# Kernel tuning notes

Measured on AMD Instinct MI355X. Metric: run time of the kernel, lower is better.

Reference implementation:

```python
import jax, jax.numpy as jnp
import numpy as np

THETA = 10000.0


def apply_rope(x, theta):
    # x: [batch, heads, seq, head_dim], head_dim even
    d = x.shape[-1]
    s = x.shape[-2]
    freqs = 1.0 / (theta ** (jnp.arange(0, d, 2, dtype=jnp.float32) / d))  # [d/2]
    pos = jnp.arange(s, dtype=jnp.float32)
    ang = pos[:, None] * freqs[None, :]          # [seq, d/2]
    cos, sin = jnp.cos(ang), jnp.sin(ang)
    x_even = x[..., 0::2]
    x_odd = x[..., 1::2]
    r_even = x_even * cos - x_odd * sin
    r_odd = x_even * sin + x_odd * cos
    # interleave back: [..., seq, d/2, 2] -> [..., seq, d]
    out = jnp.stack([r_even, r_odd], axis=-1).reshape(x.shape)
    return out


def setup_inputs() -> dict:
    key = jax.random.key(0)
    ks = jax.random.split(key, 5)
    B, S, D = 2, 2048, 1024
    scale = 1.0 / np.sqrt(D)
    return {
        "x": jax.random.normal(ks[0], (B, S, D), dtype=jnp.float32),
        "q_proj_weight": jax.random.normal(ks[1], (D, D), dtype=jnp.float32) * scale,
        "k_proj_weight": jax.random.normal(ks[2], (D, D), dtype=jnp.float32) * scale,
        "v_proj_weight": jax.random.normal(ks[3], (D, D), dtype=jnp.float32) * scale,
        "o_proj_weight": jax.random.normal(ks[4], (D, D), dtype=jnp.float32) * scale,
    }


def reference(x, q_proj_weight, k_proj_weight, v_proj_weight, o_proj_weight):
    B, S, D = x.shape
    H = 16
    hd = D // H
    # projections: weight is (d_out, d_in)
    q = jnp.einsum('bsd,ed->bse', x, q_proj_weight)
    k = jnp.einsum('bsd,ed->bse', x, k_proj_weight)
    v = jnp.einsum('bsd,ed->bse', x, v_proj_weight)
    # split heads -> [B, H, S, hd]
    q = q.reshape(B, S, H, hd).transpose(0, 2, 1, 3)
    k = k.reshape(B, S, H, hd).transpose(0, 2, 1, 3)
    v = v.reshape(B, S, H, hd).transpose(0, 2, 1, 3)
    q = apply_rope(q, THETA)
    k = apply_rope(k, THETA)
    scores = jnp.einsum('bhqd,bhkd->bhqk', q, k) / jnp.sqrt(jnp.float32(hd))
    causal = jnp.tril(jnp.ones((S, S), dtype=bool))
    scores = jnp.where(causal, scores, -jnp.inf)
    attn = jax.nn.softmax(scores, axis=-1)
    out = jnp.einsum('bhqk,bhkd->bhqd', attn, v)
    out = out.transpose(0, 2, 1, 3).reshape(B, S, D)
    return jnp.einsum('bsv,dv->bsd', out, o_proj_weight)
```

## Files before the change

kernel.cpp:

```cpp
#include <hip/hip_runtime.h>
#include <hip/hip_bf16.h>
#include <stdint.h>

typedef __attribute__((ext_vector_type(4))) float f32x4;
typedef __attribute__((ext_vector_type(8))) __bf16 bf16x8;
typedef __attribute__((ext_vector_type(4))) __bf16 bf16x4;

#define DEVI __device__ __forceinline__

static constexpr int S_  = 2048;
static constexpr int D_  = 1024;
static constexpr int H_  = 16;
static constexpr int HD_ = 64;
static constexpr int M_  = 2 * S_;
static constexpr float SCL2 = 0.18033688f;

DEVI void gload_lds16(const void* gsrc, void* ldst) {
  __builtin_amdgcn_global_load_lds(
      (__attribute__((address_space(1))) void*)(void*)gsrc,
      (__attribute__((address_space(3))) void*)ldst, 16, 0, 0);
}

DEVI float fexp2(float x) {
  float r;
  asm("v_exp_f32 %0, %1" : "=v"(r) : "v"(x));
  return r;
}

__global__ __launch_bounds__(256) void cvt_all_kernel(
    const float* __restrict__ x, const float* __restrict__ wq,
    const float* __restrict__ wk, const float* __restrict__ wv,
    const float* __restrict__ wo,
    __bf16* __restrict__ xb, __bf16* __restrict__ wqb,
    __bf16* __restrict__ wkb, __bf16* __restrict__ wvb,
    __bf16* __restrict__ wob, float* __restrict__ tab) {
  int blk = blockIdx.x;
  if (blk < 8192) {
    int i = blk * 256 + threadIdx.x;
    const float* src; __bf16* dst; int off;
    if (i < (1 << 20))                      { src = x;  dst = xb;  off = 0; }
    else if (i < (1 << 20) + (1 << 18))     { src = wq; dst = wqb; off = (1 << 20); }
    else if (i < (1 << 20) + 2 * (1 << 18)) { src = wk; dst = wkb; off = (1 << 20) + (1 << 18); }
    else if (i < (1 << 20) + 3 * (1 << 18)) { src = wv; dst = wvb; off = (1 << 20) + 2 * (1 << 18); }
    else                                    { src = wo; dst = wob; off = (1 << 20) + 3 * (1 << 18); }
    int j = i - off;
    float4 v = reinterpret_cast<const float4*>(src)[j];
    bf16x4 o;
    o[0] = (__bf16)v.x; o[1] = (__bf16)v.y; o[2] = (__bf16)v.z; o[3] = (__bf16)v.w;
    reinterpret_cast<bf16x4*>(dst)[j] = o;
  } else {
    int i = (blk - 8192) * 256 + threadIdx.x;
    int s = i >> 5, f = i & 31;
    float freq = powf(10000.0f, -(float)(2 * f) / (float)HD_);
    float ang = (float)s * freq;
    tab[2 * i]     = cosf(ang);
    tab[2 * i + 1] = sinf(ang);
  }
}

__global__ __launch_bounds__(512, 6) void gemm_qkv(
    const __bf16* __restrict__ A, const __bf16* __restrict__ W0,
    const __bf16* __restrict__ W1, const __bf16* __restrict__ W2,
    __bf16* __restrict__ Cq, __bf16* __restrict__ Ck, __bf16* __restrict__ Cvt,
    const float* __restrict__ tab) {
  __shared__ __attribute__((aligned(16))) __bf16 As[128 * 32];
  __shared__ __attribute__((aligned(16))) __bf16 Bs[128 * 32];
  const int tid  = threadIdx.x;
  const int lane = tid & 63;
  const int wv   = tid >> 6;
  const int wr   = wv >> 2;
  const int wc   = wv & 3;
  const int m0 = blockIdx.x * 128;
  const int n0 = blockIdx.y * 128;
  const int z  = blockIdx.z;
  const __bf16* W = (z == 0) ? W0 : (z == 1 ? W1 : W2);
  const int arow = lane & 15;
  const int kgrp = (lane >> 4) * 8;

  f32x4 acc[4][2];
#pragma unroll
  for (int i = 0; i < 4; i++)
#pragma unroll
    for (int j = 0; j < 2; j++) acc[i][j] = f32x4{0.f, 0.f, 0.f, 0.f};

  for (int k0 = 0; k0 < 1024; k0 += 32) {
    __syncthreads();
    {
      int c   = wv * 64 + lane;
      int row = c >> 2;
      int kc  = (c & 3) * 8;
      gload_lds16(A + (size_t)(m0 + row) * 1024 + k0 + kc, As + wv * 512);
      gload_lds16(W + (size_t)(n0 + row) * 1024 + k0 + kc, Bs + wv * 512);
    }
    asm volatile("s_waitcnt vmcnt(0)" ::: "memory");
    __syncthreads();
    bf16x8 af[4], bw[2];
#pragma unroll
    for (int i = 0; i < 4; i++)
      af[i] = *reinterpret_cast<const bf16x8*>(As + (wr * 64 + i * 16 + arow) * 32 + kgrp);
#pragma unroll
    for (int j = 0; j < 2; j++)
      bw[j] = *reinterpret_cast<const bf16x8*>(Bs + (wc * 32 + j * 16 + arow) * 32 + kgrp);
#pragma unroll
    for (int i = 0; i < 4; i++)
#pragma unroll
      for (int j = 0; j < 2; j++)
        acc[i][j] = __builtin_amdgcn_mfma_f32_16x16x32_bf16(af[i], bw[j], acc[i][j], 0, 0, 0);
  }

  if (z == 2) {
#pragma unroll
    for (int i = 0; i < 4; i++) {
      int m = m0 + wr * 64 + i * 16 + (lane >> 4) * 4;
      int bb = m >> 11, srow = m & (S_ - 1);
#pragma unroll
      for (int j = 0; j < 2; j++) {
        int n = n0 + wc * 32 + j * 16 + arow;
        int h = n >> 6, d = n & 63;
        bf16x4 o4;
#pragma unroll
        for (int r = 0; r < 4; r++) o4[r] = (__bf16)acc[i][j][r];
        *reinterpret_cast<bf16x4*>(
            Cvt + ((size_t)(bb * H_ + h) * HD_ + d) * S_ + srow) = o4;
      }
    }
  } else {
#pragma unroll
    for (int i = 0; i < 4; i++) {
#pragma unroll
      for (int j = 0; j < 2; j++) {
#pragma unroll
        for (int r = 0; r < 4; r++) {
          int m = m0 + wr * 64 + i * 16 + (lane >> 4) * 4 + r;
          int n = n0 + wc * 32 + j * 16 + arow;
          float v = acc[i][j][r];
          int bb = m >> 11, srow = m & (S_ - 1);
          int h = n >> 6, d = n & 63;
          size_t oidx = ((size_t)(bb * H_ + h) * S_ + srow) * HD_ + d;
          float other = __shfl_xor(v, 1, 64);
          int fq = d >> 1;
          float2 cssn = *reinterpret_cast<const float2*>(tab + (srow * 32 + fq) * 2);
          float rv = (d & 1) ? (other * cssn.y + v * cssn.x)
                             : (v * cssn.x - other * cssn.y);
          if (z == 0) rv *= SCL2;
          ((z == 0) ? Cq : Ck)[oidx] = (__bf16)rv;
        }
      }
    }
  }
}

__global__ __launch_bounds__(512, 4) void gemm_bt0(
    const __bf16* __restrict__ A, const __bf16* __restrict__ W0,
    float* __restrict__ Cf) {
  __shared__ __attribute__((aligned(16))) __bf16 As[128 * 32];
  __shared__ __attribute__((aligned(16))) __bf16 Bs[64 * 32];
  const int tid  = threadIdx.x;
  const int lane = tid & 63;
  const int wv   = tid >> 6;
  const int wr   = wv >> 1;
  const int wc   = wv & 1;
  const int m0 = blockIdx.x * 128;
  const int n0 = blockIdx.y * 64;
  const int arow = lane & 15;
  const int kgrp = (lane >> 4) * 8;

  f32x4 acc[2][2];
#pragma unroll
  for (int i = 0; i < 2; i++)
#pragma unroll
    for (int j = 0; j < 2; j++) acc[i][j] = f32x4{0.f, 0.f, 0.f, 0.f};

  for (int k0 = 0; k0 < 1024; k0 += 32) {
    __syncthreads();
    {
      int c   = wv * 64 + lane;
      int row = c >> 2;
      int kc  = (c & 3) * 8;
      gload_lds16(A + (size_t)(m0 + row) * 1024 + k0 + kc, As + wv * 512);
      if (wv < 4)
        gload_lds16(W0 + (size_t)(n0 + row) * 1024 + k0 + kc, Bs + wv * 512);
    }
    asm volatile("s_waitcnt vmcnt(0)" ::: "memory");
    __syncthreads();
    bf16x8 af[2], bw[2];
#pragma unroll
    for (int i = 0; i < 2; i++)
      af[i] = *reinterpret_cast<const bf16x8*>(As + (wr * 32 + i * 16 + arow) * 32 + kgrp);
#pragma unroll
    for (int j = 0; j < 2; j++)
      bw[j] = *reinterpret_cast<const bf16x8*>(Bs + (wc * 32 + j * 16 + arow) * 32 + kgrp);
#pragma unroll
    for (int i = 0; i < 2; i++)
#pragma unroll
      for (int j = 0; j < 2; j++)
        acc[i][j] = __builtin_amdgcn_mfma_f32_16x16x32_bf16(af[i], bw[j], acc[i][j], 0, 0, 0);
  }

#pragma unroll
  for (int i = 0; i < 2; i++)
#pragma unroll
    for (int j = 0; j < 2; j++)
#pragma unroll
      for (int r = 0; r < 4; r++) {
        int m = m0 + wr * 32 + i * 16 + (lane >> 4) * 4 + r;
        int n = n0 + wc * 32 + j * 16 + arow;
        Cf[(size_t)m * D_ + n] = acc[i][j][r];
      }
}

__global__ __launch_bounds__(512, 4) void attn_kernel(
    const __bf16* __restrict__ Q, const __bf16* __restrict__ K,
    const __bf16* __restrict__ Vt, __bf16* __restrict__ O) {
  __shared__ __attribute__((aligned(16))) __bf16 Ks[2][128 * 64];
  __shared__ __attribute__((aligned(16))) __bf16 Vs[2][64 * 128];
  const int tid = threadIdx.x, lane = tid & 63, wv = tid >> 6;
  const int id   = blockIdx.x;
  const int half = id >> 8;
  const int sub  = id & 255;
  const int bh   = sub & 31;
  const int pr   = sub >> 5;
  const int qt   = half ? pr : 15 - pr;
  const int b = bh >> 4, h = bh & 15;
  const __bf16* Qb  = Q  + (size_t)bh * S_ * HD_;
  const __bf16* Kb  = K  + (size_t)bh * S_ * HD_;
  const __bf16* Vtb = Vt + (size_t)bh * HD_ * S_;
  const int arow = lane & 15, g = lane >> 4;

#define STAGE(K0, BK_, BV_)                                                   \
  do {                                                                        \
    _Pragma("unroll") for (int j = 0; j < 2; ++j) {                           \
      int c = (wv * 2 + j) * 64 + lane;                    \
      int rowk = c >> 3, qqk = c & 7;                                         \
      int qsk = qqk ^ (rowk & 7);                                             \
      int ctp = rowk >> 4, rw = rowk & 15;                                    \
      int kph = ((ctp & 4) << 4) + ((ctp & 2) << 4) + ((ctp & 1) << 2)        \
                + ((rw >> 2) << 3) + (rw & 3);                                \
      gload_lds16(Kb + (size_t)((K0) + kph) * HD_ + qsk * 8,                  \
                  (BK_) + (size_t)(wv * 2 + j) * 512);                        \
      int rowv = c >> 4, qqv = c & 15;                                        \
      int qsv = qqv ^ (rowv & 7);                                             \
      gload_lds16(Vtb + (size_t)rowv * S_ + (K0) + qsv * 8,                   \
                  (BV_) + (size_t)(wv * 2 + j) * 512);                        \
    }                                                                         \
  } while (0)

  const int q0 = qt * 128;
  const int nkv = qt + 1;
  const int qw = q0 + wv * 16;
  const int qg = qw + arow;

  bf16x8 aq[2];
#pragma unroll
  for (int j = 0; j < 2; j++)
    aq[j] = *reinterpret_cast<const bf16x8*>(
        Qb + (size_t)(qw + arow) * HD_ + j * 32 + g * 8);

  f32x4 po[4];
#pragma unroll
  for (int dt = 0; dt < 4; dt++) po[dt] = f32x4{0.f, 0.f, 0.f, 0.f};
  float mrow = -1e30f, lrow = 0.f;

  STAGE(0, Ks[0], Vs[0]);
  {
    int t1 = (nkv > 1) ? 128 : 0;
    STAGE(t1, Ks[1], Vs[1]);
  }
  asm volatile("s_waitcnt vmcnt(4)" ::: "memory");
  __builtin_amdgcn_s_barrier();

  for (int kt = 0; kt < nkv; ++kt) {
    const int k0 = kt * 128;
    const int cur = kt & 1;
    const __bf16* Kc = Ks[cur];
    const __bf16* Vc = Vs[cur];

    f32x4 sc4[8];
    __builtin_amdgcn_s_setprio(1);
#pragma unroll
    for (int ct = 0; ct < 8; ct++) {
      sc4[ct] = f32x4{0.f, 0.f, 0.f, 0.f};
      int L = ct * 16 + arow;
#pragma unroll
      for (int j2 = 0; j2 < 2; j2++) {
        int byt = (L * 128 + j2 * 64 + g * 16) ^ ((L & 7) << 4);
        bf16x8 kb = *reinterpret_cast<const bf16x8*>((const char*)Kc + byt);
        sc4[ct] = __builtin_amdgcn_mfma_f32_16x16x32_bf16(kb, aq[j2], sc4[ct], 0, 0, 0);
      }
    }
    __builtin_amdgcn_s_setprio(0);

    if (kt == nkv - 1) {
#pragma unroll
      for (int ct = 0; ct < 8; ct++) {
        int kb0 = k0 + ((ct & 4) << 4) + ((ct & 2) << 4) + ((ct & 1) << 2) + g * 8;
#pragma unroll
        for (int r = 0; r < 4; r++)
          if (kb0 + r > qg) sc4[ct][r] = -1e30f;
      }
    }

    float mc[8];
#pragma unroll
    for (int ct = 0; ct < 8; ct++)
      mc[ct] = fmaxf(fmaxf(sc4[ct][0], sc4[ct][1]),
                     fmaxf(sc4[ct][2], sc4[ct][3]));
#pragma unroll
    for (int sstep = 4; sstep > 0; sstep >>= 1)
#pragma unroll
      for (int ct = 0; ct < sstep; ct++) mc[ct] = fmaxf(mc[ct], mc[ct + sstep]);
    float mx = mc[0];
    mx = fmaxf(mx, __shfl_xor(mx, 16, 64));
    mx = fmaxf(mx, __shfl_xor(mx, 32, 64));

    bool noskip = !__all(mx <= mrow + 11.0f);
    if (noskip) {
      float mnew = fmaxf(mrow, mx);
      float corr = fexp2(mrow - mnew);
      mrow = mnew;
      lrow *= corr;
#pragma unroll
      for (int dt = 0; dt < 4; dt++)
#pragma unroll
        for (int r = 0; r < 4; r++) po[dt][r] *= corr;
    }

    float rc[8];
#pragma unroll
    for (int ct = 0; ct < 8; ct++) {
      float e0 = fexp2(sc4[ct][0] - mrow);
      float e1 = fexp2(sc4[ct][1] - mrow);
      float e2 = fexp2(sc4[ct][2] - mrow);
      float e3 = fexp2(sc4[ct][3] - mrow);
      sc4[ct][0] = e0; sc4[ct][1] = e1; sc4[ct][2] = e2; sc4[ct][3] = e3;
      rc[ct] = (e0 + e1) + (e2 + e3);
    }
#pragma unroll
    for (int sstep = 4; sstep > 0; sstep >>= 1)
#pragma unroll
      for (int ct = 0; ct < sstep; ct++) rc[ct] += rc[ct + sstep];
    float rs = rc[0];
    rs += __shfl_xor(rs, 16, 64);
    rs += __shfl_xor(rs, 32, 64);
    lrow += rs;

    bf16x8 pb[4];
#pragma unroll
    for (int h2 = 0; h2 < 2; h2++)
#pragma unroll
      for (int j2 = 0; j2 < 2; j2++) {
#pragma unroll
        for (int r = 0; r < 4; r++) {
          pb[h2 * 2 + j2][r]     = (__bf16)sc4[h2 * 4 + 2 * j2][r];
          pb[h2 * 2 + j2][4 + r] = (__bf16)sc4[h2 * 4 + 2 * j2 + 1][r];
        }
      }

    __builtin_amdgcn_s_setprio(1);
#pragma unroll
    for (int dt = 0; dt < 4; dt++) {
      int d = dt * 16 + arow;
#pragma unroll
      for (int jj = 0; jj < 4; jj++) {
        int byv = (d * 256 + jj * 64 + g * 16) ^ ((d & 7) << 4);
        bf16x8 vb = *reinterpret_cast<const bf16x8*>((const char*)Vc + byv);
        po[dt] = __builtin_amdgcn_mfma_f32_16x16x32_bf16(vb, pb[jj], po[dt], 0, 0, 0);
      }
    }
    __builtin_amdgcn_s_setprio(0);

    __builtin_amdgcn_s_barrier();
    if (kt < nkv - 1) {
      int nx = kt + 2;
      if (nx > nkv - 1) nx = nkv - 1;
      STAGE(nx * 128, Ks[cur], Vs[cur]);
      asm volatile("s_waitcnt vmcnt(4)" ::: "memory");
    } else {
      asm volatile("s_waitcnt vmcnt(0)" ::: "memory");
    }
    __builtin_amdgcn_s_barrier();
  }

  float inv = __builtin_amdgcn_rcpf(lrow);
#pragma unroll
  for (int dt = 0; dt < 4; dt++) {
    bf16x4 o4;
#pragma unroll
    for (int r = 0; r < 4; r++) o4[r] = (__bf16)(po[dt][r] * inv);
    *reinterpret_cast<bf16x4*>(
        O + (size_t)(b * S_ + qg) * D_ + h * HD_ + dt * 16 + g * 4) = o4;
  }
#undef STAGE
}

extern "C" void kernel_launch(void* const* d_in, const int* in_sizes, int n_in,
                              void* d_out, int out_size, void* d_ws, size_t ws_size,
                              hipStream_t stream) {
  const float* x  = (const float*)d_in[0];
  const float* wq = (const float*)d_in[1];
  const float* wk = (const float*)d_in[2];
  const float* wv = (const float*)d_in[3];
  const float* wo = (const float*)d_in[4];
  float* out = (float*)d_out;

  char* w = (char*)d_ws;
  __bf16* xb  = (__bf16*)(w);
  __bf16* wqb = (__bf16*)(w + (8u  << 20));
  __bf16* wkb = (__bf16*)(w + (10u << 20));
  __bf16* wvb = (__bf16*)(w + (12u << 20));
  __bf16* wob = (__bf16*)(w + (14u << 20));
  __bf16* qws = (__bf16*)(w + (16u << 20));
  __bf16* kws = (__bf16*)(w + (24u << 20));
  __bf16* vtw = (__bf16*)(w + (32u << 20));
  __bf16* aws = (__bf16*)(w + (40u << 20));
  float*  tab = (float*)(w + (48u << 20));

  cvt_all_kernel<<<8448, 256, 0, stream>>>(x, wq, wk, wv, wo,
                                           xb, wqb, wkb, wvb, wob, tab);
  gemm_qkv<<<dim3(32, 8, 3), 512, 0, stream>>>(xb, wqb, wkb, wvb,
                                               qws, kws, vtw, tab);
  attn_kernel<<<512, 512, 0, stream>>>(qws, kws, vtw, aws);
  gemm_bt0<<<dim3(M_ / 128, D_ / 64), 512, 0, stream>>>(aws, wob, out);
}
```

Before: 107.4 us.

## Drop LDS staging in attention, read K/V directly from global per wave

The attention kernel no longer stages K and V tiles in shared memory with async global-to-LDS loads and barriers. Each wave now reads K and V fragments straight from global memory (relying on caches) and handles its own 16-row query tile. Each wave processes two tiles paired from opposite ends of the causal range to balance work. Blocks shrink to 256 threads on a 32x16 grid. This removes the barrier synchronisation and the LDS traffic, but loses the sharing of K/V loads between waves and exposes global-load latency with no prefetch.

```diff
diff --git a/kernel.cpp b/kernel.cpp
--- a/kernel.cpp
+++ b/kernel.cpp
@@ -209,188 +209,143 @@
       }
 }
 
-__global__ __launch_bounds__(512, 4) void attn_kernel(
+__global__ __launch_bounds__(256, 4) void attn_kernel(
     const __bf16* __restrict__ Q, const __bf16* __restrict__ K,
     const __bf16* __restrict__ Vt, __bf16* __restrict__ O) {
-  __shared__ __attribute__((aligned(16))) __bf16 Ks[2][128 * 64];
-  __shared__ __attribute__((aligned(16))) __bf16 Vs[2][64 * 128];
   const int tid = threadIdx.x, lane = tid & 63, wv = tid >> 6;
-  const int id   = blockIdx.x;
-  const int half = id >> 8;
-  const int sub  = id & 255;
-  const int bh   = sub & 31;
-  const int pr   = sub >> 5;
-  const int qt   = half ? pr : 15 - pr;
+  const int bh = blockIdx.x;
+  const int pr = blockIdx.y;
   const int b = bh >> 4, h = bh & 15;
   const __bf16* Qb  = Q  + (size_t)bh * S_ * HD_;
   const __bf16* Kb  = K  + (size_t)bh * S_ * HD_;
   const __bf16* Vtb = Vt + (size_t)bh * HD_ * S_;
   const int arow = lane & 15, g = lane >> 4;
-
-#define STAGE(K0, BK_, BV_)                                                   \
-  do {                                                                        \
-    _Pragma("unroll") for (int j = 0; j < 2; ++j) {                           \
-      int c = (wv * 2 + j) * 64 + lane;                    \
-      int rowk = c >> 3, qqk = c & 7;                                         \
-      int qsk = qqk ^ (rowk & 7);                                             \
-      int ctp = rowk >> 4, rw = rowk & 15;                                    \
-      int kph = ((ctp & 4) << 4) + ((ctp & 2) << 4) + ((ctp & 1) << 2)        \
-                + ((rw >> 2) << 3) + (rw & 3);                                \
-      gload_lds16(Kb + (size_t)((K0) + kph) * HD_ + qsk * 8,                  \
-                  (BK_) + (size_t)(wv * 2 + j) * 512);                        \
-      int rowv = c >> 4, qqv = c & 15;                                        \
-      int qsv = qqv ^ (rowv & 7);                                             \
-      gload_lds16(Vtb + (size_t)rowv * S_ + (K0) + qsv * 8,                   \
-                  (BV_) + (size_t)(wv * 2 + j) * 512);                        \
-    }                                                                         \
-  } while (0)
-
-  const int q0 = qt * 128;
-  const int nkv = qt + 1;
-  const int qw = q0 + wv * 16;
-  const int qg = qw + arow;
-
-  bf16x8 aq[2];
-#pragma unroll
-  for (int j = 0; j < 2; j++)
-    aq[j] = *reinterpret_cast<const bf16x8*>(
-        Qb + (size_t)(qw + arow) * HD_ + j * 32 + g * 8);
-
-  f32x4 po[4];
-#pragma unroll
-  for (int dt = 0; dt < 4; dt++) po[dt] = f32x4{0.f, 0.f, 0.f, 0.f};
-  float mrow = -1e30f, lrow = 0.f;
-
-  STAGE(0, Ks[0], Vs[0]);
-  {
-    int t1 = (nkv > 1) ? 128 : 0;
-    STAGE(t1, Ks[1], Vs[1]);
-  }
-  asm volatile("s_waitcnt vmcnt(4)" ::: "memory");
-  __builtin_amdgcn_s_barrier();
-
-  for (int kt = 0; kt < nkv; ++kt) {
-    const int k0 = kt * 128;
-    const int cur = kt & 1;
-    const __bf16* Kc = Ks[cur];
-    const __bf16* Vc = Vs[cur];
-
-    f32x4 sc4[8];
-    __builtin_amdgcn_s_setprio(1);
-#pragma unroll
-    for (int ct = 0; ct < 8; ct++) {
-      sc4[ct] = f32x4{0.f, 0.f, 0.f, 0.f};
-      int L = ct * 16 + arow;
-#pragma unroll
-      for (int j2 = 0; j2 < 2; j2++) {
-        int byt = (L * 128 + j2 * 64 + g * 16) ^ ((L & 7) << 4);
-        bf16x8 kb = *reinterpret_cast<const bf16x8*>((const char*)Kc + byt);
-        sc4[ct] = __builtin_amdgcn_mfma_f32_16x16x32_bf16(kb, aq[j2], sc4[ct], 0, 0, 0);
-      }
-    }
-    __builtin_amdgcn_s_setprio(0);
-
-    if (kt == nkv - 1) {
+  const int kprm = ((arow >> 2) << 3) + (arow & 3);
+
+  for (int seg = 0; seg < 2; ++seg) {
+    const int t = (seg == 0) ? (pr * 4 + wv) : (127 - pr * 4 - wv);
+    const int q0 = t * 16;
+    const int nkv = (t >> 3) + 1;
+    const int qg = q0 + arow;
+
+    bf16x8 aq[2];
+#pragma unroll
+    for (int j = 0; j < 2; j++)
+      aq[j] = *reinterpret_cast<const bf16x8*>(
+          Qb + (size_t)(q0 + arow) * HD_ + j * 32 + g * 8);
+
+    f32x4 po[4];
+#pragma unroll
+    for (int dt = 0; dt < 4; dt++) po[dt] = f32x4{0.f, 0.f, 0.f, 0.f};
+    float mrow = -1e30f, lrow = 0.f;
+
+    for (int kt = 0; kt < nkv; ++kt) {
+      const int k0 = kt * 128;
+
+      f32x4 sc4[8];
+      __builtin_amdgcn_s_setprio(1);
 #pragma unroll
       for (int ct = 0; ct < 8; ct++) {
-        int kb0 = k0 + ((ct & 4) << 4) + ((ct & 2) << 4) + ((ct & 1) << 2) + g * 8;
-#pragma unroll
-        for (int r = 0; r < 4; r++)
-          if (kb0 + r > qg) sc4[ct][r] = -1e30f;
-      }
-    }
-
-    float mc[8];
-#pragma unroll
-    for (int ct = 0; ct < 8; ct++)
-      mc[ct] = fmaxf(fmaxf(sc4[ct][0], sc4[ct][1]),
-                     fmaxf(sc4[ct][2], sc4[ct][3]));
-#pragma unroll
-    for (int sstep = 4; sstep > 0; sstep >>= 1)
-#pragma unroll
-      for (int ct = 0; ct < sstep; ct++) mc[ct] = fmaxf(mc[ct], mc[ct + sstep]);
-    float mx = mc[0];
-    mx = fmaxf(mx, __shfl_xor(mx, 16, 64));
-    mx = fmaxf(mx, __shfl_xor(mx, 32, 64));
-
-    bool noskip = !__all(mx <= mrow + 11.0f);
-    if (noskip) {
-      float mnew = fmaxf(mrow, mx);
-      float corr = fexp2(mrow - mnew);
-      mrow = mnew;
-      lrow *= corr;
-#pragma unroll
-      for (int dt = 0; dt < 4; dt++)
-#pragma unroll
-        for (int r = 0; r < 4; r++) po[dt][r] *= corr;
-    }
-
-    float rc[8];
-#pragma unroll
-    for (int ct = 0; ct < 8; ct++) {
-      float e0 = fexp2(sc4[ct][0] - mrow);
-      float e1 = fexp2(sc4[ct][1] - mrow);
-      float e2 = fexp2(sc4[ct][2] - mrow);
-      float e3 = fexp2(sc4[ct][3] - mrow);
-      sc4[ct][0] = e0; sc4[ct][1] = e1; sc4[ct][2] = e2; sc4[ct][3] = e3;
-      rc[ct] = (e0 + e1) + (e2 + e3);
-    }
-#pragma unroll
-    for (int sstep = 4; sstep > 0; sstep >>= 1)
-#pragma unroll
-      for (int ct = 0; ct < sstep; ct++) rc[ct] += rc[ct + sstep];
-    float rs = rc[0];
-    rs += __shfl_xor(rs, 16, 64);
-    rs += __shfl_xor(rs, 32, 64);
-    lrow += rs;
-
-    bf16x8 pb[4];
-#pragma unroll
-    for (int h2 = 0; h2 < 2; h2++)
-#pragma unroll
-      for (int j2 = 0; j2 < 2; j2++) {
-#pragma unroll
-        for (int r = 0; r < 4; r++) {
-          pb[h2 * 2 + j2][r]     = (__bf16)sc4[h2 * 4 + 2 * j2][r];
-          pb[h2 * 2 + j2][4 + r] = (__bf16)sc4[h2 * 4 + 2 * j2 + 1][r];
-        }
-      }
-
-    __builtin_amdgcn_s_setprio(1);
+        sc4[ct] = f32x4{0.f, 0.f, 0.f, 0.f};
+        int base = ((ct & 4) << 4) + ((ct & 2) << 4) + ((ct & 1) << 2);
+        const __bf16* kr = Kb + (size_t)(k0 + base + kprm) * HD_ + g * 8;
+#pragma unroll
+        for (int j2 = 0; j2 < 2; j2++) {
+          bf16x8 kb = *reinterpret_cast<const bf16x8*>(kr + j2 * 32);
+          sc4[ct] = __builtin_amdgcn_mfma_f32_16x16x32_bf16(kb, aq[j2], sc4[ct], 0, 0, 0);
+        }
+      }
+      __builtin_amdgcn_s_setprio(0);
+
+      if (kt == nkv - 1) {
+#pragma unroll
+        for (int ct = 0; ct < 8; ct++) {
+          int kb0 = k0 + ((ct & 4) << 4) + ((ct & 2) << 4) + ((ct & 1) << 2) + g * 8;
+#pragma unroll
+          for (int r = 0; r < 4; r++)
+            if (kb0 + r > qg) sc4[ct][r] = -1e30f;
+        }
+      }
+
+      float mc[8];
+#pragma unroll
+      for (int ct = 0; ct < 8; ct++)
+        mc[ct] = fmaxf(fmaxf(sc4[ct][0], sc4[ct][1]),
+                       fmaxf(sc4[ct][2], sc4[ct][3]));
+#pragma unroll
+      for (int sstep = 4; sstep > 0; sstep >>= 1)
+#pragma unroll
+        for (int ct = 0; ct < sstep; ct++) mc[ct] = fmaxf(mc[ct], mc[ct + sstep]);
+      float mx = mc[0];
+      mx = fmaxf(mx, __shfl_xor(mx, 16, 64));
+      mx = fmaxf(mx, __shfl_xor(mx, 32, 64));
+
+      bool noskip = !__all(mx <= mrow + 11.0f);
+      if (noskip) {
+        float mnew = fmaxf(mrow, mx);
+        float corr = fexp2(mrow - mnew);
+        mrow = mnew;
+        lrow *= corr;
+#pragma unroll
+        for (int dt = 0; dt < 4; dt++)
+#pragma unroll
+          for (int r = 0; r < 4; r++) po[dt][r] *= corr;
+      }
+
+      float rc[8];
+#pragma unroll
+      for (int ct = 0; ct < 8; ct++) {
+        float e0 = fexp2(sc4[ct][0] - mrow);
+        float e1 = fexp2(sc4[ct][1] - mrow);
+        float e2 = fexp2(sc4[ct][2] - mrow);
+        float e3 = fexp2(sc4[ct][3] - mrow);
+        sc4[ct][0] = e0; sc4[ct][1] = e1; sc4[ct][2] = e2; sc4[ct][3] = e3;
+        rc[ct] = (e0 + e1) + (e2 + e3);
+      }
+#pragma unroll
+      for (int sstep = 4; sstep > 0; sstep >>= 1)
+#pragma unroll
+        for (int ct = 0; ct < sstep; ct++) rc[ct] += rc[ct + sstep];
+      float rs = rc[0];
+      rs += __shfl_xor(rs, 16, 64);
+      rs += __shfl_xor(rs, 32, 64);
+      lrow += rs;
+
+      bf16x8 pb[4];
+#pragma unroll
+      for (int h2 = 0; h2 < 2; h2++)
+#pragma unroll
+        for (int j2 = 0; j2 < 2; j2++) {
+#pragma unroll
+          for (int r = 0; r < 4; r++) {
+            pb[h2 * 2 + j2][r]     = (__bf16)sc4[h2 * 4 + 2 * j2][r];
+            pb[h2 * 2 + j2][4 + r] = (__bf16)sc4[h2 * 4 + 2 * j2 + 1][r];
+          }
+        }
+
+      __builtin_amdgcn_s_setprio(1);
+#pragma unroll
+      for (int dt = 0; dt < 4; dt++) {
+        const __bf16* vr = Vtb + (size_t)(dt * 16 + arow) * S_ + k0 + g * 8;
+#pragma unroll
+        for (int jj = 0; jj < 4; jj++) {
+          bf16x8 vb = *reinterpret_cast<const bf16x8*>(vr + jj * 32);
+          po[dt] = __builtin_amdgcn_mfma_f32_16x16x32_bf16(vb, pb[jj], po[dt], 0, 0, 0);
+        }
+      }
+      __builtin_amdgcn_s_setprio(0);
+    }
+
+    float inv = __builtin_amdgcn_rcpf(lrow);
 #pragma unroll
     for (int dt = 0; dt < 4; dt++) {
-      int d = dt * 16 + arow;
-#pragma unroll
-      for (int jj = 0; jj < 4; jj++) {
-        int byv = (d * 256 + jj * 64 + g * 16) ^ ((d & 7) << 4);
-        bf16x8 vb = *reinterpret_cast<const bf16x8*>((const char*)Vc + byv);
-        po[dt] = __builtin_amdgcn_mfma_f32_16x16x32_bf16(vb, pb[jj], po[dt], 0, 0, 0);
-      }
-    }
-    __builtin_amdgcn_s_setprio(0);
-
-    __builtin_amdgcn_s_barrier();
-    if (kt < nkv - 1) {
-      int nx = kt + 2;
-      if (nx > nkv - 1) nx = nkv - 1;
-      STAGE(nx * 128, Ks[cur], Vs[cur]);
-      asm volatile("s_waitcnt vmcnt(4)" ::: "memory");
-    } else {
-      asm volatile("s_waitcnt vmcnt(0)" ::: "memory");
-    }
-    __builtin_amdgcn_s_barrier();
-  }
-
-  float inv = __builtin_amdgcn_rcpf(lrow);
-#pragma unroll
-  for (int dt = 0; dt < 4; dt++) {
-    bf16x4 o4;
-#pragma unroll
-    for (int r = 0; r < 4; r++) o4[r] = (__bf16)(po[dt][r] * inv);
-    *reinterpret_cast<bf16x4*>(
-        O + (size_t)(b * S_ + qg) * D_ + h * HD_ + dt * 16 + g * 4) = o4;
-  }
-#undef STAGE
+      bf16x4 o4;
+#pragma unroll
+      for (int r = 0; r < 4; r++) o4[r] = (__bf16)(po[dt][r] * inv);
+      *reinterpret_cast<bf16x4*>(
+          O + (size_t)(b * S_ + qg) * D_ + h * HD_ + dt * 16 + g * 4) = o4;
+    }
+  }
 }
 
 extern "C" void kernel_launch(void* const* d_in, const int* in_sizes, int n_in,
@@ -419,6 +374,6 @@
                                            xb, wqb, wkb, wvb, wob, tab);
   gemm_qkv<<<dim3(32, 8, 3), 512, 0, stream>>>(xb, wqb, wkb, wvb,
                                                qws, kws, vtw, tab);
-  attn_kernel<<<512, 512, 0, stream>>>(qws, kws, vtw, aws);
+  attn_kernel<<<dim3(32, 16), 256, 0, stream>>>(qws, kws, vtw, aws);
   gemm_bt0<<<dim3(M_ / 128, D_ / 64), 512, 0, stream>>>(aws, wob, out);
 }
```

New measurement: 190.7 us. +77.6%, slower.
